# Optimization experiments

Measured on AMD Instinct MI355X. Metric: run time of the kernel, lower is better.

The kernel has to match this reference:

```python
import jax, jax.numpy as jnp
import numpy as np

N, IN_DIM, OUT_DIM = 4096, 512, 512
H, D = 8, OUT_DIM // 8          # num_heads, head_dim
ALPHA = 0.2                     # leaky relu slope
NEG = -9e15
EPS = 1e-5


def setup_inputs() -> dict:
    key = jax.random.key(0)
    k1, k2, k3, k4 = jax.random.split(key, 4)
    x = jax.random.normal(k1, (N, IN_DIM), dtype=jnp.float32)
    adj = jax.random.randint(k2, (N, N), 0, 2, dtype=jnp.int32)
    # scale params like nn.Linear default init (~1/sqrt(fan_in)) to keep scores sane
    W = jax.random.normal(k3, (OUT_DIM, IN_DIM), dtype=jnp.float32) / np.sqrt(IN_DIM)
    a = jax.random.normal(k4, (2 * D,), dtype=jnp.float32) / np.sqrt(2 * D)
    gamma = jnp.ones((OUT_DIM,), dtype=jnp.float32)
    beta = jnp.zeros((OUT_DIM,), dtype=jnp.float32)
    return {"x": x, "adj": adj, "W": W, "a": a, "gamma": gamma, "beta": beta}


def reference(x, adj, W, a, gamma, beta):
    n = x.shape[0]
    Wh = (x @ W.T).reshape(n, H, D)                       # [N, H, D]
    a_src, a_dst = a[:D], a[D:]                           # shared across heads
    s_src = jnp.einsum('jhd,d->jh', Wh, a_src)            # [N, H] source term
    s_dst = jnp.einsum('ihd,d->ih', Wh, a_dst)            # [N, H] dest term
    # e[i, j, h] = leakyrelu(a_src . Wh[j,h] + a_dst . Wh[i,h]); row i = dst, col j = src
    e = jax.nn.leaky_relu(s_dst[:, None, :] + s_src[None, :, :], negative_slope=ALPHA)
    e = jnp.where((adj > 0)[:, :, None], e, NEG)          # mask non-edges
    attn = jax.nn.softmax(e, axis=1)                      # softmax over source nodes j
    h_prime = jnp.einsum('ijh,jhd->ihd', attn, Wh).reshape(n, H * D)  # [N, out_dim]
    # BatchNorm1d (training-mode batch statistics, biased variance)
    mean = jnp.mean(h_prime, axis=0)
    var = jnp.var(h_prime, axis=0)
    h_prime = gamma * (h_prime - mean) * jax.lax.rsqrt(var + EPS) + beta
    return jax.nn.relu(h_prime)
```

## Files before the change

kernel.cpp:

```cpp
#include <hip/hip_runtime.h>
#include <hip/hip_bf16.h>
#include <hip/hip_fp16.h>
#include <stdint.h>


typedef __attribute__((ext_vector_type(4))) float f32x4;
typedef __attribute__((ext_vector_type(8))) short s16x8;
typedef __attribute__((ext_vector_type(2))) _Float16 h2v;

#define LOG2E 1.4426950408889634f

static __device__ __forceinline__ ushort f2bf(float f) {
  union { float f; uint32_t u; } v; v.f = f;
  uint32_t r = (v.u + 0x7FFFu + ((v.u >> 16) & 1u)) >> 16;
  return (ushort)r;
}

static __device__ __forceinline__ short bf16b(float f) {
  __hip_bfloat16 h = __float2bfloat16(f);
  union { __hip_bfloat16 h; short s; } c; c.h = h;
  return c.s;
}

static __device__ __forceinline__ float bf2f(ushort u) {
  union { uint32_t u; float f; } c; c.u = ((uint32_t)u) << 16;
  return c.f;
}

static __device__ __forceinline__ ushort hbits(float f) {
  union { _Float16 h; ushort u; } c; c.h = (_Float16)f;
  return c.u;
}

static __device__ __forceinline__ h2v u2h2(uint32_t u) {
  union { uint32_t u; h2v h; } c; c.u = u; return c.h;
}
static __device__ __forceinline__ uint32_t h22u(h2v h) {
  union { uint32_t u; h2v h; } c; c.h = h; return c.u;
}

static __device__ __forceinline__ uint32_t mask2f16(uint32_t w, int q) {
#if __has_builtin(__builtin_amdgcn_sbfe) && __has_builtin(__builtin_amdgcn_perm)
  const uint32_t mlo = (uint32_t)__builtin_amdgcn_sbfe((int)w, q, 1);
  const uint32_t mhi = (uint32_t)__builtin_amdgcn_sbfe((int)w, q + 1, 1);
  return __builtin_amdgcn_perm(mhi, mlo, 0x07060100u);
#else
  return (((w >> q) & 1u) | (((w >> q) & 2u) << 15)) * 0xFFFFu;
#endif
}

static __device__ __forceinline__ void gl_lds16(const ushort* g, ushort* l) {
  __builtin_amdgcn_global_load_lds(
      (const __attribute__((address_space(1))) unsigned int*)(g),
      (__attribute__((address_space(3))) unsigned int*)(l), 16, 0, 0);
}

__global__ __launch_bounds__(256) void k_prep(const float* __restrict__ x,
                                              const float* __restrict__ W,
                                              const int* __restrict__ adj,
                                              ushort* __restrict__ xb,
                                              ushort* __restrict__ wb,
                                              unsigned long long* __restrict__ maskw,
                                              float* __restrict__ stats) {
  const int t = threadIdx.x;
  if (blockIdx.x < 2304) {
    const int idx = (blockIdx.x * 256 + t) * 4;
    const int NX = 4096 * 512;
    if (idx < NX) {
      float4 v = *(const float4*)(x + idx);
      ushort4 o; o.x = f2bf(v.x); o.y = f2bf(v.y); o.z = f2bf(v.z); o.w = f2bf(v.w);
      *(ushort4*)(xb + idx) = o;
    } else {
      const int k = idx - NX;
      float4 v = *(const float4*)(W + k);
      ushort4 o; o.x = f2bf(v.x); o.y = f2bf(v.y); o.z = f2bf(v.z); o.w = f2bf(v.w);
      *(ushort4*)(wb + k) = o;
    }
  } else {
    const int pb = blockIdx.x - 2304;
    if (pb == 0) {
      stats[t] = 0.f; stats[t + 256] = 0.f; stats[t + 512] = 0.f; stats[t + 768] = 0.f;
    }
    const size_t base = (size_t)pb * 8192;
    const int lane = t & 63;
#pragma unroll 4
    for (int it = 0; it < 32; ++it) {
      const size_t elem = base + it * 256 + t;
      unsigned long long b = __ballot(adj[elem] > 0);
      if (lane == 0) maskw[elem >> 6] = b;
    }
  }
}

__global__ __launch_bounds__(256) void k_gemm(const ushort* __restrict__ xb,
                                              const ushort* __restrict__ wb,
                                              const float* __restrict__ a,
                                              ushort* __restrict__ WhT,
                                              ushort* __restrict__ EsT,
                                              ushort* __restrict__ es2T,
                                              float* __restrict__ rT) {
  __shared__ ushort bt[64 * 512];
  float* tl = (float*)bt;
  const int lane = threadIdx.x & 63;
  const int wv = threadIdx.x >> 6;
  const int l15 = lane & 15, lg = lane >> 4;
  const int m0 = blockIdx.x * 64;
  const int h = blockIdx.y;
  const int n0 = h * 64;

#pragma unroll
  for (int it = 0; it < 16; ++it) {
    const int col = it * 4 + wv;
    const ushort* src = wb + (size_t)(n0 + col) * 512 + (lane ^ (col & 7)) * 8;
    gl_lds16(src, &bt[col * 512]);
  }
  __syncthreads();

  const ushort* ap = xb + (size_t)(m0 + wv * 16 + l15) * 512 + lg * 8;
  f32x4 acc[4] = {};
  for (int k0 = 0; k0 < 512; k0 += 32) {
    s16x8 av = *(const s16x8*)(ap + k0);
#pragma unroll
    for (int ct = 0; ct < 4; ++ct) {
      const int col = ct * 16 + l15;
      s16x8 b = *(const s16x8*)((const char*)bt + col * 1024 +
                                (((k0 + lg * 8) * 2) ^ ((col & 7) << 4)));
      acc[ct] = __builtin_amdgcn_mfma_f32_16x16x32_bf16(av, b, acc[ct], 0, 0, 0);
    }
  }
  float aS[4], aD[4];
#pragma unroll
  for (int ct = 0; ct < 4; ++ct) {
    aS[ct] = a[ct * 16 + l15];
    aD[ct] = a[64 + ct * 16 + l15];
  }
#pragma unroll
  for (int r = 0; r < 4; ++r) {
    float s1 = acc[0][r] * aS[0] + acc[1][r] * aS[1] + acc[2][r] * aS[2] + acc[3][r] * aS[3];
    float s2 = acc[0][r] * aD[0] + acc[1][r] * aD[1] + acc[2][r] * aD[2] + acc[3][r] * aD[3];
#pragma unroll
    for (int off = 1; off < 16; off <<= 1) {
      s1 += __shfl_xor(s1, off);
      s2 += __shfl_xor(s2, off);
    }
    if (l15 == 0) {
      const int row = m0 + wv * 16 + lg * 4 + r;
      const float aa = s1 * LOG2E;
      const float bb = s2 * LOG2E;
      EsT[h * 4096 + row]  = hbits(__builtin_amdgcn_exp2f(aa));
      es2T[h * 4096 + row] = hbits(__builtin_amdgcn_exp2f(0.2f * aa));
      rT[h * 4096 + row]   = __builtin_amdgcn_exp2f(-0.8f * bb);
    }
  }
  __syncthreads();
#pragma unroll
  for (int ct = 0; ct < 4; ++ct)
#pragma unroll
    for (int r = 0; r < 4; ++r)
      tl[(ct * 16 + l15) * 65 + wv * 16 + lg * 4 + r] = acc[ct][r];
  __syncthreads();
  const int c = threadIdx.x >> 2, mb = (threadIdx.x & 3) * 16;
  s16x8 o0, o1;
#pragma unroll
  for (int k = 0; k < 8; ++k) o0[k] = (short)hbits(tl[c * 65 + mb + k]);
#pragma unroll
  for (int k = 0; k < 8; ++k) o1[k] = (short)hbits(tl[c * 65 + mb + 8 + k]);
  *(s16x8*)(WhT + (size_t)(n0 + c) * 4096 + m0 + mb) = o0;
  *(s16x8*)(WhT + (size_t)(n0 + c) * 4096 + m0 + mb + 8) = o1;
}

__global__ __launch_bounds__(512, 4) void k_attn(
    const uint32_t* __restrict__ mask32,
    const ushort* __restrict__ WhT,
    const ushort* __restrict__ EsT,
    const ushort* __restrict__ es2T,
    const float* __restrict__ rT,
    ushort* __restrict__ num,
    float* __restrict__ lbuf) {
  __shared__ ushort tile[4][4096];
  __shared__ uint32_t mask_s[256 * 33];
  __shared__ uint32_t Es_s[512];
  __shared__ uint32_t es2_s[512];

  const int t = threadIdx.x;
  const int lane = t & 63, wv = t >> 6;
  const int l15 = lane & 15, lg = lane >> 4;
  const int h = blockIdx.y;
  const int jh = blockIdx.x & 3;
  const int ih = blockIdx.x >> 2;
  const int i0b = ih * 256;
  const int j0 = jh * 1024;

  if (t < 128) {
    ((uint4*)Es_s)[t] = ((const uint4*)EsT)[(h * 4096 + j0) / 8 + t];
  } else if (t < 256) {
    ((uint4*)es2_s)[t - 128] = ((const uint4*)es2T)[(h * 4096 + j0) / 8 + t - 128];
  }
  {
    const int r = t >> 1, part = t & 1;
    const uint32_t* src = mask32 + (size_t)(i0b + r) * 128 + jh * 32 + part * 16;
    uint32_t* dst = &mask_s[r * 33 + part * 16];
#pragma unroll
    for (int k = 0; k < 4; ++k)
      *(int4*)(dst + k * 4) = *(const int4*)(src + k * 4);
  }
  const int cg = (wv << 3) + (lane >> 3);
  const int gg = (lane & 7) ^ (cg & 7);
  const ushort* sbase = WhT + (size_t)(h * 64 + cg) * 4096 + j0 + gg * 8;

  gl_lds16(sbase, &tile[0][wv * 512]);
  gl_lds16(sbase + 64, &tile[1][wv * 512]);
  gl_lds16(sbase + 128, &tile[2][wv * 512]);
  __syncthreads();

  const int rloc = wv * 32 + l15;
  const float r0f = rT[h * 4096 + i0b + rloc];
  const float r1f = rT[h * 4096 + i0b + rloc + 16];
  const h2v r02 = {(_Float16)r0f, (_Float16)r0f};
  const h2v r12 = {(_Float16)r1f, (_Float16)r1f};

  f32x4 acc[2][4] = {};
  f32x4 accd0 = {}, accd1 = {};
  s16x8 bones;
  {
    const short v = (l15 == 0) ? (short)0x3C00 : (short)0;
    bones[0] = v; bones[1] = v; bones[2] = v; bones[3] = v;
    bones[4] = v; bones[5] = v; bones[6] = v; bones[7] = v;
  }

#pragma unroll 1
  for (int c = 0; c < 16; ++c) {
    if (c < 14)       asm volatile("s_waitcnt vmcnt(2)" ::: "memory");
    else if (c == 14) asm volatile("s_waitcnt vmcnt(1)" ::: "memory");
    else              asm volatile("s_waitcnt vmcnt(0)" ::: "memory");
    __builtin_amdgcn_s_barrier();
    if (c < 13) gl_lds16(sbase + (size_t)(c + 3) * 64, &tile[(c + 3) & 3][wv * 512]);
    const char* tb = (const char*)&tile[c & 3][0];
#pragma unroll
    for (int half = 0; half < 2; ++half) {
      const int jsub = half * 32;
      const uint4 e4 = *(const uint4*)&Es_s[c * 32 + (jsub >> 1) + lg * 4];
      const uint4 f4 = *(const uint4*)&es2_s[c * 32 + (jsub >> 1) + lg * 4];
      const uint32_t w0 = mask_s[rloc * 33 + c * 2 + half] >> (lg * 8);
      const uint32_t w1 = mask_s[(rloc + 16) * 33 + c * 2 + half] >> (lg * 8);
      s16x8 b[4];
#pragma unroll
      for (int ct = 0; ct < 4; ++ct) {
        const int col = ct * 16 + l15;
        b[ct] = *(const s16x8*)(tb + col * 128 + ((jsub * 2 + lg * 16) ^ ((col & 7) << 4)));
      }
      union { s16x8 v8; uint32_t u32[4]; } pa0, pa1;
#pragma unroll
      for (int q2 = 0; q2 < 4; ++q2) {
        const int q = q2 * 2;
        const h2v e2 = u2h2(((const uint32_t*)&e4)[q2]);
        const h2v f2 = u2h2(((const uint32_t*)&f4)[q2]);
        const h2v t0 = __builtin_elementwise_max(e2, r02 * f2);
        const h2v t1 = __builtin_elementwise_max(e2, r12 * f2);
        pa0.u32[q2] = mask2f16(w0, q) & h22u(t0);
        pa1.u32[q2] = mask2f16(w1, q) & h22u(t1);
      }
      accd0 = __builtin_amdgcn_mfma_f32_16x16x32_f16(pa0.v8, bones, accd0, 0, 0, 0);
      accd1 = __builtin_amdgcn_mfma_f32_16x16x32_f16(pa1.v8, bones, accd1, 0, 0, 0);
#pragma unroll
      for (int ct = 0; ct < 4; ++ct) {
        acc[0][ct] = __builtin_amdgcn_mfma_f32_16x16x32_f16(pa0.v8, b[ct], acc[0][ct], 0, 0, 0);
        acc[1][ct] = __builtin_amdgcn_mfma_f32_16x16x32_f16(pa1.v8, b[ct], acc[1][ct], 0, 0, 0);
      }
    }
  }

  if (l15 == 0) {
    float* lb = &lbuf[((size_t)jh * 8 + h) * 4096 + i0b + rloc];
#pragma unroll
    for (int r = 0; r < 4; ++r) lb[lg * 4 + r] = accd0[r];
#pragma unroll
    for (int r = 0; r < 4; ++r) lb[16 + lg * 4 + r] = accd1[r];
  }
  ushort* np = num + (size_t)jh * 4096 * 512;
#pragma unroll
  for (int rs = 0; rs < 2; ++rs)
#pragma unroll
    for (int ct = 0; ct < 4; ++ct)
#pragma unroll
      for (int r = 0; r < 4; ++r)
        np[(size_t)(i0b + wv * 32 + rs * 16 + lg * 4 + r) * 512 + h * 64 + ct * 16 + l15] =
            (ushort)bf16b(acc[rs][ct][r]);
}

__global__ __launch_bounds__(512) void k_stats(const ushort* __restrict__ num,
                                               const float* __restrict__ lbuf,
                                               ushort* __restrict__ hpb,
                                               float* __restrict__ stats) {
  __shared__ float vt[16][520];
  __shared__ float linv_s[128];
  const int t = threadIdx.x;
  const int r0 = blockIdx.x * 16;
  if (t < 128) {
    const int r = r0 + (t >> 3), hh = t & 7;
    float l = 0.f;
#pragma unroll
    for (int s = 0; s < 4; ++s) l += lbuf[((size_t)s * 8 + hh) * 4096 + r];
    linv_s[t] = 1.0f / l;
  }
  __syncthreads();
  const int r = t >> 5;
  const int c0 = (t & 31) * 16;
  const int rr = r0 + r;
  float nsum[16] = {};
#pragma unroll
  for (int s = 0; s < 4; ++s) {
    const ushort* p = num + (size_t)s * 4096 * 512 + (size_t)rr * 512 + c0;
    s16x8 a0 = *(const s16x8*)(p);
    s16x8 a1 = *(const s16x8*)(p + 8);
#pragma unroll
    for (int k = 0; k < 8; ++k) {
      nsum[k] += bf2f((ushort)a0[k]);
      nsum[8 + k] += bf2f((ushort)a1[k]);
    }
  }
  const float li = linv_s[r * 8 + (c0 >> 6)];
  s16x8 o0, o1;
#pragma unroll
  for (int k = 0; k < 16; ++k) {
    const float v = nsum[k] * li;
    vt[r][c0 + k] = v;
    if (k < 8) o0[k] = bf16b(v); else o1[k - 8] = bf16b(v);
  }
  *(s16x8*)(hpb + (size_t)rr * 512 + c0) = o0;
  *(s16x8*)(hpb + (size_t)rr * 512 + c0 + 8) = o1;
  __syncthreads();
  float s1 = 0.f, s2 = 0.f;
#pragma unroll
  for (int k = 0; k < 16; ++k) {
    const float v = vt[k][t];
    s1 += v; s2 += v * v;
  }
  atomicAdd(&stats[t], s1);
  atomicAdd(&stats[512 + t], s2);
}

__global__ __launch_bounds__(256) void k_apply(const ushort* __restrict__ hpb,
                                               const float* __restrict__ stats,
                                               const float* __restrict__ gamma,
                                               const float* __restrict__ beta,
                                               float* __restrict__ out) {
  const size_t idx8 = ((size_t)blockIdx.x * 256 + threadIdx.x) * 8;
  const int c0 = (int)(idx8 & 511);
  s16x8 hv = *(const s16x8*)(hpb + idx8);
#pragma unroll
  for (int k = 0; k < 8; ++k) {
    const int cc = c0 + k;
    const float mean = stats[cc] * (1.f / 4096.f);
    const float var = stats[512 + cc] * (1.f / 4096.f) - mean * mean;
    const float v = bf2f((ushort)hv[k]);
    const float val = (v - mean) * rsqrtf(var + 1e-5f) * gamma[cc] + beta[cc];
    out[idx8 + k] = fmaxf(val, 0.f);
  }
}

extern "C" void kernel_launch(void* const* d_in, const int* in_sizes, int n_in,
                              void* d_out, int out_size, void* d_ws, size_t ws_size,
                              hipStream_t stream) {
  const float* x = (const float*)d_in[0];
  const int* adj = (const int*)d_in[1];
  const float* W = (const float*)d_in[2];
  const float* a = (const float*)d_in[3];
  const float* gamma = (const float*)d_in[4];
  const float* beta = (const float*)d_in[5];
  float* out = (float*)d_out;

  char* ws = (char*)d_ws;
  size_t off = 0;
  auto alloc = [&](size_t bytes) -> void* {
    void* p = ws + off;
    off += (bytes + 255) & ~(size_t)255;
    return p;
  };
  ushort* WhT   = (ushort*)alloc((size_t)512 * 4096 * 2);
  ushort* EsT   = (ushort*)alloc((size_t)8 * 4096 * 2);
  ushort* es2T  = (ushort*)alloc((size_t)8 * 4096 * 2);
  float*  rT    = (float*)alloc((size_t)8 * 4096 * 4);
  unsigned long long* maskw = (unsigned long long*)alloc((size_t)4096 * 64 * 8);
  float*  lbuf  = (float*)alloc((size_t)32 * 4096 * 4);
  ushort* hpb   = (ushort*)alloc((size_t)4096 * 512 * 2);
  float*  stats = (float*)alloc((size_t)1024 * 4);
  const size_t ov = off;
  ushort* xb = (ushort*)(ws + ov);
  ushort* wb = (ushort*)(ws + ov + (size_t)4096 * 512 * 2);
  ushort* num = (ushort*)(ws + ov);

  hipLaunchKernelGGL(k_prep, dim3(4352), dim3(256), 0, stream,
                     x, W, adj, xb, wb, maskw, stats);
  hipLaunchKernelGGL(k_gemm, dim3(64, 8), dim3(256), 0, stream, xb, wb, a,
                     WhT, EsT, es2T, rT);
  hipLaunchKernelGGL(k_attn, dim3(64, 8), dim3(512), 0, stream,
                     (const uint32_t*)maskw, WhT, EsT, es2T, rT, num, lbuf);
  hipLaunchKernelGGL(k_stats, dim3(256), dim3(512), 0, stream, num, lbuf, hpb, stats);
  hipLaunchKernelGGL(k_apply, dim3(1024), dim3(256), 0, stream, hpb, stats, gamma, beta, out);
}
```

Baseline: 74.22 us.

## Move adj mask packing into GEMM launch and read W operand directly from global

The bf16 conversion of x and W now runs alone in its own kernel. The adjacency ballot-packing work moves into the GEMM launch as extra blocks, so the memory-bound mask packing can overlap with the MFMA projection blocks. The GEMM also stops staging the W tile in LDS through global_load_lds and reads B fragments straight from global memory, which shrinks LDS use. The trade-off is more redundant global and L2 traffic for the B operand, and mask blocks that compete with GEMM blocks for compute units.

```diff
diff --git a/kernel.cpp b/kernel.cpp
--- a/kernel.cpp
+++ b/kernel.cpp
@@ -55,29 +55,39 @@
       (__attribute__((address_space(3))) unsigned int*)(l), 16, 0, 0);
 }
 
-__global__ __launch_bounds__(256) void k_prep(const float* __restrict__ x,
+__global__ __launch_bounds__(256) void k_conv(const float* __restrict__ x,
                                               const float* __restrict__ W,
-                                              const int* __restrict__ adj,
                                               ushort* __restrict__ xb,
-                                              ushort* __restrict__ wb,
-                                              unsigned long long* __restrict__ maskw,
-                                              float* __restrict__ stats) {
+                                              ushort* __restrict__ wb) {
+  const int idx = (blockIdx.x * 256 + threadIdx.x) * 4;
+  const int NX = 4096 * 512;
+  if (idx < NX) {
+    float4 v = *(const float4*)(x + idx);
+    ushort4 o; o.x = f2bf(v.x); o.y = f2bf(v.y); o.z = f2bf(v.z); o.w = f2bf(v.w);
+    *(ushort4*)(xb + idx) = o;
+  } else {
+    const int k = idx - NX;
+    float4 v = *(const float4*)(W + k);
+    ushort4 o; o.x = f2bf(v.x); o.y = f2bf(v.y); o.z = f2bf(v.z); o.w = f2bf(v.w);
+    *(ushort4*)(wb + k) = o;
+  }
+}
+
+__global__ __launch_bounds__(256) void k_pack_gemm(
+    const int* __restrict__ adj,
+    const ushort* __restrict__ xb,
+    const ushort* __restrict__ wb,
+    const float* __restrict__ a,
+    unsigned long long* __restrict__ maskw,
+    float* __restrict__ stats,
+    ushort* __restrict__ WhT,
+    ushort* __restrict__ EsT,
+    ushort* __restrict__ es2T,
+    float* __restrict__ rT) {
+  __shared__ float tl[64 * 65];
   const int t = threadIdx.x;
-  if (blockIdx.x < 2304) {
-    const int idx = (blockIdx.x * 256 + t) * 4;
-    const int NX = 4096 * 512;
-    if (idx < NX) {
-      float4 v = *(const float4*)(x + idx);
-      ushort4 o; o.x = f2bf(v.x); o.y = f2bf(v.y); o.z = f2bf(v.z); o.w = f2bf(v.w);
-      *(ushort4*)(xb + idx) = o;
-    } else {
-      const int k = idx - NX;
-      float4 v = *(const float4*)(W + k);
-      ushort4 o; o.x = f2bf(v.x); o.y = f2bf(v.y); o.z = f2bf(v.z); o.w = f2bf(v.w);
-      *(ushort4*)(wb + k) = o;
-    }
-  } else {
-    const int pb = blockIdx.x - 2304;
+  if (blockIdx.x < 2048) {
+    const int pb = blockIdx.x;
     if (pb == 0) {
       stats[t] = 0.f; stats[t + 256] = 0.f; stats[t + 512] = 0.f; stats[t + 768] = 0.f;
     }
@@ -89,32 +99,15 @@
       unsigned long long b = __ballot(adj[elem] > 0);
       if (lane == 0) maskw[elem >> 6] = b;
     }
-  }
-}
-
-__global__ __launch_bounds__(256) void k_gemm(const ushort* __restrict__ xb,
-                                              const ushort* __restrict__ wb,
-                                              const float* __restrict__ a,
-                                              ushort* __restrict__ WhT,
-                                              ushort* __restrict__ EsT,
-                                              ushort* __restrict__ es2T,
-                                              float* __restrict__ rT) {
-  __shared__ ushort bt[64 * 512];
-  float* tl = (float*)bt;
-  const int lane = threadIdx.x & 63;
-  const int wv = threadIdx.x >> 6;
+    return;
+  }
+  const int g = blockIdx.x - 2048;
+  const int lane = t & 63;
+  const int wv = t >> 6;
   const int l15 = lane & 15, lg = lane >> 4;
-  const int m0 = blockIdx.x * 64;
-  const int h = blockIdx.y;
+  const int m0 = (g & 63) * 64;
+  const int h = g >> 6;
   const int n0 = h * 64;
-
-#pragma unroll
-  for (int it = 0; it < 16; ++it) {
-    const int col = it * 4 + wv;
-    const ushort* src = wb + (size_t)(n0 + col) * 512 + (lane ^ (col & 7)) * 8;
-    gl_lds16(src, &bt[col * 512]);
-  }
-  __syncthreads();
 
   const ushort* ap = xb + (size_t)(m0 + wv * 16 + l15) * 512 + lg * 8;
   f32x4 acc[4] = {};
@@ -122,9 +115,7 @@
     s16x8 av = *(const s16x8*)(ap + k0);
 #pragma unroll
     for (int ct = 0; ct < 4; ++ct) {
-      const int col = ct * 16 + l15;
-      s16x8 b = *(const s16x8*)((const char*)bt + col * 1024 +
-                                (((k0 + lg * 8) * 2) ^ ((col & 7) << 4)));
+      s16x8 b = *(const s16x8*)(wb + (size_t)(n0 + ct * 16 + l15) * 512 + k0 + lg * 8);
       acc[ct] = __builtin_amdgcn_mfma_f32_16x16x32_bf16(av, b, acc[ct], 0, 0, 0);
     }
   }
@@ -152,14 +143,13 @@
       rT[h * 4096 + row]   = __builtin_amdgcn_exp2f(-0.8f * bb);
     }
   }
-  __syncthreads();
 #pragma unroll
   for (int ct = 0; ct < 4; ++ct)
 #pragma unroll
     for (int r = 0; r < 4; ++r)
       tl[(ct * 16 + l15) * 65 + wv * 16 + lg * 4 + r] = acc[ct][r];
   __syncthreads();
-  const int c = threadIdx.x >> 2, mb = (threadIdx.x & 3) * 16;
+  const int c = t >> 2, mb = (t & 3) * 16;
   s16x8 o0, o1;
 #pragma unroll
   for (int k = 0; k < 8; ++k) o0[k] = (short)hbits(tl[c * 65 + mb + k]);
@@ -390,10 +380,9 @@
   ushort* wb = (ushort*)(ws + ov + (size_t)4096 * 512 * 2);
   ushort* num = (ushort*)(ws + ov);
 
-  hipLaunchKernelGGL(k_prep, dim3(4352), dim3(256), 0, stream,
-                     x, W, adj, xb, wb, maskw, stats);
-  hipLaunchKernelGGL(k_gemm, dim3(64, 8), dim3(256), 0, stream, xb, wb, a,
-                     WhT, EsT, es2T, rT);
+  hipLaunchKernelGGL(k_conv, dim3(2304), dim3(256), 0, stream, x, W, xb, wb);
+  hipLaunchKernelGGL(k_pack_gemm, dim3(2560), dim3(256), 0, stream,
+                     adj, xb, wb, a, maskw, stats, WhT, EsT, es2T, rT);
   hipLaunchKernelGGL(k_attn, dim3(64, 8), dim3(512), 0, stream,
                      (const uint32_t*)maskw, WhT, EsT, es2T, rT, num, lbuf);
   hipLaunchKernelGGL(k_stats, dim3(256), dim3(512), 0, stream, num, lbuf, hpb, stats);
```

Measured after the change: 110.3 us. +48.6%, slower.
